# Kernel optimization log

Measured on AMD Instinct MI355X. Metric: run time of the kernel, lower is better.

The kernel has to match this reference:

```python
import jax, jax.numpy as jnp
import numpy as np

B, H, W, C = 16, 256, 256, 16
HO, WO = 256, 256


def setup_inputs() -> dict:
    key = jax.random.key(0)
    k1, k2 = jax.random.split(key)
    x = jax.random.normal(k1, (B, H, W, C), dtype=jnp.float32)
    # loc network: global avg pool -> dense(C, 6); small weights, identity bias
    W_loc = jax.random.normal(k2, (C, 6), dtype=jnp.float32) * 0.01
    b_loc = jnp.asarray([1.0, 0.0, 0.0, 1.0, 0.0, 0.0], dtype=jnp.float32)
    # coords_grid = np.indices(output_grid_shape): (2, HO, WO), [0]=row idx, [1]=col idx
    coords_grid = jnp.asarray(np.indices((HO, WO), dtype=np.float32))
    return {"x": x, "W_loc": W_loc, "b_loc": b_loc, "coords_grid": coords_grid}


def _forward(x, W_loc, b_loc, coords_grid):
    # loc network: predict 6 affine params per batch element
    pooled = jnp.mean(x, axis=(1, 2))              # [B, C]
    params = pooled @ W_loc + b_loc                # [B, 6]
    A = params[:, :4].reshape(-1, 2, 2)            # [B, 2, 2]
    t = params[:, 4:]                              # [B, 2]
    # grid_transform_fn: affine map of pixel coordinates
    tc = jnp.einsum('bij,jhw->bihw', A, coords_grid) + t[:, :, None, None]  # [B,2,HO,WO]
    yc, xc = tc[:, 0], tc[:, 1]                    # [B, HO, WO] each
    # interpolation_fn: bilinear sampling with clipping (wrap=False)
    y0 = jnp.floor(yc)
    x0 = jnp.floor(xc)
    wy = yc - y0                                   # fractional weights
    wx = xc - x0
    y0i = jnp.clip(y0.astype(jnp.int32), 0, H - 1)
    y1i = jnp.clip(y0.astype(jnp.int32) + 1, 0, H - 1)
    x0i = jnp.clip(x0.astype(jnp.int32), 0, W - 1)
    x1i = jnp.clip(x0.astype(jnp.int32) + 1, 0, W - 1)
    bidx = jnp.arange(x.shape[0])[:, None, None]   # [B,1,1] batch gather index
    Ia = x[bidx, y0i, x0i]                         # [B,HO,WO,C]
    Ib = x[bidx, y0i, x1i]
    Ic = x[bidx, y1i, x0i]
    Id = x[bidx, y1i, x1i]
    wa = ((1.0 - wy) * (1.0 - wx))[..., None]
    wb = ((1.0 - wy) * wx)[..., None]
    wc = (wy * (1.0 - wx))[..., None]
    wd = (wy * wx)[..., None]
    return wa * Ia + wb * Ib + wc * Ic + wd * Id   # [B,HO,WO,C]


def reference(x, W_loc, b_loc, coords_grid):
    return _forward(x, W_loc, b_loc, coords_grid)
```

## Files before the change

kernel.cpp:

```cpp
#include <hip/hip_runtime.h>

#define BB 16
#define HH 256
#define WW 256
#define CC 16
#define NPIX (HH * WW)
#define SLICES 128
#define POOL_BLOCKS (BB * SLICES)
#define SAMPLE_BLOCKS (BB * 128)

typedef float vf4 __attribute__((ext_vector_type(4)));

__global__ __launch_bounds__(256) void pool_partial(const float4* __restrict__ x4,
                                                    float4* __restrict__ part) {
    const int blk = blockIdx.x;
    const int tid = threadIdx.x;
    const float4* p = x4 + (size_t)blk * 2048 + tid;
    float4 acc = {0.f, 0.f, 0.f, 0.f};
#pragma unroll
    for (int k = 0; k < 8; ++k) {
        float4 v = p[k * 256];
        acc.x += v.x; acc.y += v.y; acc.z += v.z; acc.w += v.w;
    }
    for (int off = 4; off < 64; off <<= 1) {
        acc.x += __shfl_down(acc.x, off);
        acc.y += __shfl_down(acc.y, off);
        acc.z += __shfl_down(acc.z, off);
        acc.w += __shfl_down(acc.w, off);
    }
    __shared__ float4 wsum[4][4];
    const int wave = tid >> 6, lane = tid & 63;
    if (lane < 4) wsum[wave][lane] = acc;
    __syncthreads();
    if (tid < 4) {
        float4 t0 = wsum[0][tid], t1 = wsum[1][tid];
        float4 t2 = wsum[2][tid], t3 = wsum[3][tid];
        float4 t;
        t.x = t0.x + t1.x + t2.x + t3.x;
        t.y = t0.y + t1.y + t2.y + t3.y;
        t.z = t0.z + t1.z + t2.z + t3.z;
        t.w = t0.w + t1.w + t2.w + t3.w;
        part[blk * 4 + tid] = t;
    }
}

__global__ __launch_bounds__(256) void params_kernel(const float4* __restrict__ part,
                                                     const float* __restrict__ W_loc,
                                                     const float* __restrict__ b_loc,
                                                     float* __restrict__ prm) {
    const int b   = blockIdx.x;
    const int tid = threadIdx.x;
    const int wave = tid >> 6, lane = tid & 63;
    __shared__ float4 wsum[4][4];
    __shared__ float  pooled[CC];

    const float4* q = part + (size_t)b * 512;
    float4 a0 = q[tid], a1 = q[tid + 256];
    float4 acc;
    acc.x = a0.x + a1.x; acc.y = a0.y + a1.y;
    acc.z = a0.z + a1.z; acc.w = a0.w + a1.w;
    for (int off = 4; off < 64; off <<= 1) {
        acc.x += __shfl_down(acc.x, off);
        acc.y += __shfl_down(acc.y, off);
        acc.z += __shfl_down(acc.z, off);
        acc.w += __shfl_down(acc.w, off);
    }
    if (lane < 4) wsum[wave][lane] = acc;
    __syncthreads();
    if (tid < 4) {
        float4 t0 = wsum[0][tid], t1 = wsum[1][tid];
        float4 t2 = wsum[2][tid], t3 = wsum[3][tid];
        pooled[tid * 4 + 0] = (t0.x + t1.x + t2.x + t3.x) * (1.0f / 65536.0f);
        pooled[tid * 4 + 1] = (t0.y + t1.y + t2.y + t3.y) * (1.0f / 65536.0f);
        pooled[tid * 4 + 2] = (t0.z + t1.z + t2.z + t3.z) * (1.0f / 65536.0f);
        pooled[tid * 4 + 3] = (t0.w + t1.w + t2.w + t3.w) * (1.0f / 65536.0f);
    }
    __syncthreads();
    if (tid < 6) {
        float a = b_loc[tid];
#pragma unroll
        for (int c = 0; c < CC; ++c)
            a += pooled[c] * W_loc[c * 6 + tid];
        prm[b * 8 + tid] = a;
    }
}

__global__ __launch_bounds__(256) void sample_v2(const char* __restrict__ xb0,
                                                 const float* __restrict__ prm,
                                                 char* __restrict__ ob0) {
    const int tid = threadIdx.x;
    const int blk = blockIdx.x;
    const int b   = blk >> 7;

    const float* pp = prm + b * 8;
    const float p0 = pp[0], p1 = pp[1], p2 = pp[2];
    const float p3 = pp[3], p4 = pp[4], p5 = pp[5];

    const char* xb = xb0 + ((size_t)b << 22);
    char*       ob = ob0 + ((size_t)b << 22);
    const unsigned int cqo = (unsigned int)(tid & 3) << 4;

    const int pixBase = (blk & 127) * 512 + (tid >> 2);
    const int h0 = (blk & 127) * 2;
    const int w0 = tid >> 2;

#pragma unroll 4
    for (int k = 0; k < 8; ++k) {
        const int hh  = h0 + (k >> 2);
        const int wpx = w0 + ((k & 3) << 6);

        const float fh = (float)hh, fw = (float)wpx;
        const float yc = p0 * fh + p1 * fw + p4;
        const float xc = p2 * fh + p3 * fw + p5;

        const float y0f = floorf(yc), x0f = floorf(xc);
        const float wy = yc - y0f, wx = xc - x0f;
        const int y0 = (int)y0f, x0v = (int)x0f;
        const int y0i = min(max(y0,     0), HH - 1);
        const int y1i = min(max(y0 + 1, 0), HH - 1);
        const int x0i = min(max(x0v,     0), WW - 1);
        const int x1i = min(max(x0v + 1, 0), WW - 1);

        const unsigned int r0 = ((unsigned int)y0i << 14) + cqo;
        const unsigned int r1 = ((unsigned int)y1i << 14) + cqo;
        const unsigned int c0 = (unsigned int)x0i << 6;
        const unsigned int c1 = (unsigned int)x1i << 6;

        const vf4 Ia = *(const vf4*)(xb + (r0 + c0));
        const vf4 Ib = *(const vf4*)(xb + (r0 + c1));
        const vf4 Ic = *(const vf4*)(xb + (r1 + c0));
        const vf4 Id = *(const vf4*)(xb + (r1 + c1));

        const float omy = 1.f - wy, omx = 1.f - wx;
        const float wa = omy * omx, wb_ = omy * wx;
        const float wc_ = wy * omx, wd = wy * wx;

        vf4 o = wa * Ia + wb_ * Ib + wc_ * Ic + wd * Id;

        const unsigned int po = ((unsigned int)(pixBase + (k << 6)) << 6) + cqo;
        __builtin_nontemporal_store(o, (vf4*)(ob + po));
    }
}

extern "C" void kernel_launch(void* const* d_in, const int* in_sizes, int n_in,
                              void* d_out, int out_size, void* d_ws, size_t ws_size,
                              hipStream_t stream) {
    const float* x     = (const float*)d_in[0];
    const float* W_loc = (const float*)d_in[1];
    const float* b_loc = (const float*)d_in[2];

    float4* part = (float4*)d_ws;
    float*  prm  = (float*)((char*)d_ws + 2048 * 4 * sizeof(float4));

    pool_partial<<<POOL_BLOCKS, 256, 0, stream>>>((const float4*)x, part);
    params_kernel<<<BB, 256, 0, stream>>>(part, W_loc, b_loc, prm);
    sample_v2<<<SAMPLE_BLOCKS, 256, 0, stream>>>((const char*)x, prm, (char*)d_out);
}
```

Measured before the change: 133.4 us.

## Fuse affine-parameter computation into sampling kernel and halve block counts

Removes the separate params kernel. Each sampling block now reduces its batch's pooled partial sums and computes the six affine parameters itself, which saves one kernel launch and its dependency gap. Pool and sample blocks each process twice as much work (1024 blocks instead of 2048). The cost is redundant per-block reduction work, 64 blocks per batch each doing it, plus extra barriers before sampling starts.

```diff
diff --git a/kernel.cpp b/kernel.cpp
--- a/kernel.cpp
+++ b/kernel.cpp
@@ -5,9 +5,9 @@
 #define WW 256
 #define CC 16
 #define NPIX (HH * WW)
-#define SLICES 128
-#define POOL_BLOCKS (BB * SLICES)
-#define SAMPLE_BLOCKS (BB * 128)
+
+#define POOL_BLOCKS 1024
+#define SAMPLE_BLOCKS 1024
 
 typedef float vf4 __attribute__((ext_vector_type(4)));
 
@@ -15,10 +15,10 @@
                                                     float4* __restrict__ part) {
     const int blk = blockIdx.x;
     const int tid = threadIdx.x;
-    const float4* p = x4 + (size_t)blk * 2048 + tid;
+    const float4* p = x4 + (size_t)blk * 4096 + tid;
     float4 acc = {0.f, 0.f, 0.f, 0.f};
 #pragma unroll
-    for (int k = 0; k < 8; ++k) {
+    for (int k = 0; k < 16; ++k) {
         float4 v = p[k * 256];
         acc.x += v.x; acc.y += v.y; acc.z += v.z; acc.w += v.w;
     }
@@ -44,70 +44,66 @@
     }
 }
 
-__global__ __launch_bounds__(256) void params_kernel(const float4* __restrict__ part,
-                                                     const float* __restrict__ W_loc,
-                                                     const float* __restrict__ b_loc,
-                                                     float* __restrict__ prm) {
-    const int b   = blockIdx.x;
-    const int tid = threadIdx.x;
+__global__ __launch_bounds__(256) void sample_fused(
+    const char*  __restrict__ xb0,
+    const float* __restrict__ W_loc,
+    const float* __restrict__ b_loc,
+    const float4* __restrict__ part,
+    char*        __restrict__ ob0)
+{
+    const int tid  = threadIdx.x;
+    const int blk  = blockIdx.x;
+    const int b    = blk >> 6;
+    const int loc  = blk & 63;
     const int wave = tid >> 6, lane = tid & 63;
+
     __shared__ float4 wsum[4][4];
     __shared__ float  pooled[CC];
+    __shared__ float  prs[6];
 
-    const float4* q = part + (size_t)b * 512;
-    float4 a0 = q[tid], a1 = q[tid + 256];
-    float4 acc;
-    acc.x = a0.x + a1.x; acc.y = a0.y + a1.y;
-    acc.z = a0.z + a1.z; acc.w = a0.w + a1.w;
-    for (int off = 4; off < 64; off <<= 1) {
-        acc.x += __shfl_down(acc.x, off);
-        acc.y += __shfl_down(acc.y, off);
-        acc.z += __shfl_down(acc.z, off);
-        acc.w += __shfl_down(acc.w, off);
+    {
+        const float4* q = part + (size_t)b * 256;
+        float4 acc = q[tid];
+        for (int off = 4; off < 64; off <<= 1) {
+            acc.x += __shfl_down(acc.x, off);
+            acc.y += __shfl_down(acc.y, off);
+            acc.z += __shfl_down(acc.z, off);
+            acc.w += __shfl_down(acc.w, off);
+        }
+        if (lane < 4) wsum[wave][lane] = acc;
+        __syncthreads();
+        if (tid < 4) {
+            float4 t0 = wsum[0][tid], t1 = wsum[1][tid];
+            float4 t2 = wsum[2][tid], t3 = wsum[3][tid];
+            pooled[tid * 4 + 0] = (t0.x + t1.x + t2.x + t3.x) * (1.0f / 65536.0f);
+            pooled[tid * 4 + 1] = (t0.y + t1.y + t2.y + t3.y) * (1.0f / 65536.0f);
+            pooled[tid * 4 + 2] = (t0.z + t1.z + t2.z + t3.z) * (1.0f / 65536.0f);
+            pooled[tid * 4 + 3] = (t0.w + t1.w + t2.w + t3.w) * (1.0f / 65536.0f);
+        }
+        __syncthreads();
+        if (tid < 6) {
+            float a = b_loc[tid];
+#pragma unroll
+            for (int c = 0; c < CC; ++c)
+                a += pooled[c] * W_loc[c * 6 + tid];
+            prs[tid] = a;
+        }
+        __syncthreads();
     }
-    if (lane < 4) wsum[wave][lane] = acc;
-    __syncthreads();
-    if (tid < 4) {
-        float4 t0 = wsum[0][tid], t1 = wsum[1][tid];
-        float4 t2 = wsum[2][tid], t3 = wsum[3][tid];
-        pooled[tid * 4 + 0] = (t0.x + t1.x + t2.x + t3.x) * (1.0f / 65536.0f);
-        pooled[tid * 4 + 1] = (t0.y + t1.y + t2.y + t3.y) * (1.0f / 65536.0f);
-        pooled[tid * 4 + 2] = (t0.z + t1.z + t2.z + t3.z) * (1.0f / 65536.0f);
-        pooled[tid * 4 + 3] = (t0.w + t1.w + t2.w + t3.w) * (1.0f / 65536.0f);
-    }
-    __syncthreads();
-    if (tid < 6) {
-        float a = b_loc[tid];
-#pragma unroll
-        for (int c = 0; c < CC; ++c)
-            a += pooled[c] * W_loc[c * 6 + tid];
-        prm[b * 8 + tid] = a;
-    }
-}
 
-__global__ __launch_bounds__(256) void sample_v2(const char* __restrict__ xb0,
-                                                 const float* __restrict__ prm,
-                                                 char* __restrict__ ob0) {
-    const int tid = threadIdx.x;
-    const int blk = blockIdx.x;
-    const int b   = blk >> 7;
-
-    const float* pp = prm + b * 8;
-    const float p0 = pp[0], p1 = pp[1], p2 = pp[2];
-    const float p3 = pp[3], p4 = pp[4], p5 = pp[5];
+    const float p0 = prs[0], p1 = prs[1], p2 = prs[2];
+    const float p3 = prs[3], p4 = prs[4], p5 = prs[5];
 
     const char* xb = xb0 + ((size_t)b << 22);
     char*       ob = ob0 + ((size_t)b << 22);
     const unsigned int cqo = (unsigned int)(tid & 3) << 4;
-
-    const int pixBase = (blk & 127) * 512 + (tid >> 2);
-    const int h0 = (blk & 127) * 2;
-    const int w0 = tid >> 2;
+    const int pixBase = loc * 1024 + (tid >> 2);
 
 #pragma unroll 4
-    for (int k = 0; k < 8; ++k) {
-        const int hh  = h0 + (k >> 2);
-        const int wpx = w0 + ((k & 3) << 6);
+    for (int k = 0; k < 16; ++k) {
+        const int pix = pixBase + k * 64;
+        const int hh  = pix >> 8;
+        const int wpx = pix & 255;
 
         const float fh = (float)hh, fw = (float)wpx;
         const float yc = p0 * fh + p1 * fw + p4;
@@ -137,7 +133,7 @@
 
         vf4 o = wa * Ia + wb_ * Ib + wc_ * Ic + wd * Id;
 
-        const unsigned int po = ((unsigned int)(pixBase + (k << 6)) << 6) + cqo;
+        const unsigned int po = ((unsigned int)pix << 6) + cqo;
         __builtin_nontemporal_store(o, (vf4*)(ob + po));
     }
 }
@@ -150,9 +146,8 @@
     const float* b_loc = (const float*)d_in[2];
 
     float4* part = (float4*)d_ws;
-    float*  prm  = (float*)((char*)d_ws + 2048 * 4 * sizeof(float4));
 
     pool_partial<<<POOL_BLOCKS, 256, 0, stream>>>((const float4*)x, part);
-    params_kernel<<<BB, 256, 0, stream>>>(part, W_loc, b_loc, prm);
-    sample_v2<<<SAMPLE_BLOCKS, 256, 0, stream>>>((const char*)x, prm, (char*)d_out);
+    sample_fused<<<SAMPLE_BLOCKS, 256, 0, stream>>>((const char*)x, W_loc, b_loc,
+                                                    part, (char*)d_out);
 }
```

Measured after the change: 127.4 us. 1.05x faster.
